# Kernel tuning notes

Hardware: AMD Instinct MI355X
Metric: run time of the kernel (lower is better)

The kernel has to match this reference:

```python
import jax, jax.numpy as jnp
import numpy as np

B, T, N = 64, 100, 20000
ALPHA, BETA = 1.0, 0.5  # ExpRelu params


def setup_inputs() -> dict:
    rng = np.random.default_rng(0)
    # Proper SE(3) poses so the inverse is well-conditioned
    A = rng.normal(size=(B, 3, 3))
    Q, _ = np.linalg.qr(A)
    det = np.linalg.det(Q)
    Q[:, :, 0] *= det[:, None]  # force det(R) = +1
    poses = np.tile(np.eye(4, dtype=np.float64), (B, 1, 1))
    poses[:, :3, :3] = Q
    poses[:, :3, 3] = rng.normal(size=(B, 3)) * 10.0
    # Homogeneous global boundary points [4, N]
    pts = rng.normal(size=(3, N)) * 50.0
    boundary = np.concatenate([pts, np.ones((1, N))], axis=0)
    # Unit boundary normals [3, N]
    nrm = rng.normal(size=(3, N))
    nrm /= np.linalg.norm(nrm, axis=0, keepdims=True)
    # Local-frame waypoints [B, T, 3]
    wpts = rng.normal(size=(B, T, 3)) * 5.0
    return {
        "posesglobal": jnp.asarray(poses, dtype=jnp.float32),
        "waypointslocal": jnp.asarray(wpts, dtype=jnp.float32),
        "boundary": jnp.asarray(boundary, dtype=jnp.float32),
        "boundarynormals": jnp.asarray(nrm, dtype=jnp.float32),
    }


def _exp_relu(x):
    return jnp.where(x > 0.0, ALPHA * x + 1.0, jnp.exp(BETA * x))


def reference(posesglobal, waypointslocal, boundary, boundarynormals):
    posesinv = jnp.linalg.inv(posesglobal)                     # [B,4,4]
    # boundary points into each local frame: [B,N,3]
    bpl = jnp.einsum("bij,jn->bni", posesinv, boundary)[..., :3]
    # rotate normals into local frame: [B,N,3]
    bnl = jnp.einsum("bij,jn->bni", posesinv[:, :3, :3], boundarynormals)
    # 1-NN search: squared distances [B,T,N] (argmin-equivalent to cdist)
    w2 = jnp.sum(waypointslocal * waypointslocal, axis=-1)     # [B,T]
    p2 = jnp.sum(bpl * bpl, axis=-1)                           # [B,N]
    cross = jnp.einsum("btd,bnd->btn", waypointslocal, bpl)    # [B,T,N]
    d2 = w2[:, :, None] + p2[:, None, :] - 2.0 * cross
    idx = jnp.argmin(d2, axis=2)                               # [B,T]
    cp = jnp.take_along_axis(bpl, idx[..., None], axis=1)      # [B,T,3]
    cn = jnp.take_along_axis(bnl, idx[..., None], axis=1)      # [B,T,3]
    dots = jnp.sum((waypointslocal - cp) * cn, axis=2)         # [B,T]
    loss = jnp.mean(jnp.mean(_exp_relu(dots), axis=1))         # scalar
    return loss
```

## Files before the change

kernel.cpp:

```cpp
#include <hip/hip_runtime.h>
#include <math.h>
#include <float.h>

#define B_ 64
#define T_ 100
#define N_ 20000
#define NQ (B_ * T_)
#define NCHUNKS 100
#define CHUNK (N_ / NCHUNKS)
#define PAIRS (CHUNK / 2)
#define GROUPS (PAIRS / 2)
#define QG 256
#define NQG (NQ / QG)
#define K1_THREADS 128

typedef float f2 __attribute__((ext_vector_type(2)));
typedef float f4 __attribute__((ext_vector_type(4)));
typedef unsigned long long u64;

#define KEYS_OFF 0

__device__ __forceinline__ unsigned int f32_sortable(float f) {
    unsigned int u = __float_as_uint(f);
    return ((int)u >= 0) ? (u | 0x80000000u) : ~u;
}

__global__ __launch_bounds__(256) void k0_init(u64* __restrict__ keys,
                                               float* __restrict__ out)
{
    const int i = blockIdx.x * 256 + threadIdx.x;
    keys[i] = ~0ull;
    if (i == 0) out[0] = 0.0f;
}

__global__ __launch_bounds__(K1_THREADS) void k1_nn(
    const float* __restrict__ poses,
    const float* __restrict__ wpts,
    const float* __restrict__ boundary,
    u64* __restrict__ keys)
{
    __shared__ f4 sh[PAIRS][2];
    const int bx   = blockIdx.x;
    const int qg   = bx / NCHUNKS;
    const int c    = bx - qg * NCHUNKS;
    const int base = c * CHUNK;
    const int tid  = threadIdx.x;

    if (tid < PAIRS) {
        const int p  = tid;
        const int n0 = base + 2 * p;
        const float x0 = boundary[n0],          x1 = boundary[n0 + 1];
        const float y0 = boundary[N_ + n0],     y1 = boundary[N_ + n0 + 1];
        const float z0 = boundary[2 * N_ + n0], z1 = boundary[2 * N_ + n0 + 1];
        f4 a = { -2.f * x0, -2.f * x1, -2.f * y0, -2.f * y1 };
        f4 b = { -2.f * z0, -2.f * z1,
                 x0 * x0 + y0 * y0 + z0 * z0,
                 x1 * x1 + y1 * y1 + z1 * z1 };
        sh[p][0] = a;
        sh[p][1] = b;
    }

    const int i0 = qg * QG + tid;
    const int i1 = i0 + K1_THREADS;

    float q0x, q0y, q0z, q1x, q1y, q1z;
    {
        int b0 = i0 / T_;
        const float* P = poses + b0 * 16;
        const float* W = wpts + i0 * 3;
        float wx = W[0], wy = W[1], wz = W[2];
        q0x = P[0] * wx + P[1] * wy + P[2]  * wz + P[3];
        q0y = P[4] * wx + P[5] * wy + P[6]  * wz + P[7];
        q0z = P[8] * wx + P[9] * wy + P[10] * wz + P[11];
    }
    {
        int b1 = i1 / T_;
        const float* P = poses + b1 * 16;
        const float* W = wpts + i1 * 3;
        float wx = W[0], wy = W[1], wz = W[2];
        q1x = P[0] * wx + P[1] * wy + P[2]  * wz + P[3];
        q1y = P[4] * wx + P[5] * wy + P[6]  * wz + P[7];
        q1z = P[8] * wx + P[9] * wy + P[10] * wz + P[11];
    }
    __syncthreads();

    const f2 v0x = { q0x, q0x }, v0y = { q0y, q0y }, v0z = { q0z, q0z };
    const f2 v1x = { q1x, q1x }, v1y = { q1y, q1y }, v1z = { q1z, q1z };

    float best0 = FLT_MAX, best1 = FLT_MAX;
    int   bg0 = 0, bg1 = 0;

#pragma unroll 5
    for (int g = 0; g < GROUPS; ++g) {
        const f4 a0 = sh[2 * g][0],     b0 = sh[2 * g][1];
        const f4 a1 = sh[2 * g + 1][0], b1 = sh[2 * g + 1][1];
        const f2 mx0 = { a0.x, a0.y }, my0 = { a0.z, a0.w };
        const f2 mz0 = { b0.x, b0.y }, p20 = { b0.z, b0.w };
        const f2 mx1 = { a1.x, a1.y }, my1 = { a1.z, a1.w };
        const f2 mz1 = { b1.x, b1.y }, p21 = { b1.z, b1.w };

        f2 eA = __builtin_elementwise_fma(mx0, v0x,
                __builtin_elementwise_fma(my0, v0y,
                __builtin_elementwise_fma(mz0, v0z, p20)));
        f2 eB = __builtin_elementwise_fma(mx1, v0x,
                __builtin_elementwise_fma(my1, v0y,
                __builtin_elementwise_fma(mz1, v0z, p21)));
        float m0 = fminf(fminf(eA.x, eA.y), fminf(eB.x, eB.y));
        if (m0 < best0) { best0 = m0; bg0 = g; }

        f2 eC = __builtin_elementwise_fma(mx0, v1x,
                __builtin_elementwise_fma(my0, v1y,
                __builtin_elementwise_fma(mz0, v1z, p20)));
        f2 eD = __builtin_elementwise_fma(mx1, v1x,
                __builtin_elementwise_fma(my1, v1y,
                __builtin_elementwise_fma(mz1, v1z, p21)));
        float m1 = fminf(fminf(eC.x, eC.y), fminf(eD.x, eD.y));
        if (m1 < best1) { best1 = m1; bg1 = g; }
    }

    {
        const f4 a0 = sh[2 * bg0][0],     b0 = sh[2 * bg0][1];
        const f4 a1 = sh[2 * bg0 + 1][0], b1 = sh[2 * bg0 + 1][1];
        const f2 mx0 = { a0.x, a0.y }, my0 = { a0.z, a0.w };
        const f2 mz0 = { b0.x, b0.y }, p20 = { b0.z, b0.w };
        const f2 mx1 = { a1.x, a1.y }, my1 = { a1.z, a1.w };
        const f2 mz1 = { b1.x, b1.y }, p21 = { b1.z, b1.w };
        f2 eA = __builtin_elementwise_fma(mx0, v0x,
                __builtin_elementwise_fma(my0, v0y,
                __builtin_elementwise_fma(mz0, v0z, p20)));
        f2 eB = __builtin_elementwise_fma(mx1, v0x,
                __builtin_elementwise_fma(my1, v0y,
                __builtin_elementwise_fma(mz1, v0z, p21)));
        int loc = 4 * bg0;
        int li = (eA.x == best0) ? loc
               : (eA.y == best0) ? loc + 1
               : (eB.x == best0) ? loc + 2 : loc + 3;
        u64 key = ((u64)f32_sortable(best0) << 32) | (unsigned)(base + li);
        atomicMin(&keys[i0], key);
    }
    {
        const f4 a0 = sh[2 * bg1][0],     b0 = sh[2 * bg1][1];
        const f4 a1 = sh[2 * bg1 + 1][0], b1 = sh[2 * bg1 + 1][1];
        const f2 mx0 = { a0.x, a0.y }, my0 = { a0.z, a0.w };
        const f2 mz0 = { b0.x, b0.y }, p20 = { b0.z, b0.w };
        const f2 mx1 = { a1.x, a1.y }, my1 = { a1.z, a1.w };
        const f2 mz1 = { b1.x, b1.y }, p21 = { b1.z, b1.w };
        f2 eC = __builtin_elementwise_fma(mx0, v1x,
                __builtin_elementwise_fma(my0, v1y,
                __builtin_elementwise_fma(mz0, v1z, p20)));
        f2 eD = __builtin_elementwise_fma(mx1, v1x,
                __builtin_elementwise_fma(my1, v1y,
                __builtin_elementwise_fma(mz1, v1z, p21)));
        int loc = 4 * bg1;
        int li = (eC.x == best1) ? loc
               : (eC.y == best1) ? loc + 1
               : (eD.x == best1) ? loc + 2 : loc + 3;
        u64 key = ((u64)f32_sortable(best1) << 32) | (unsigned)(base + li);
        atomicMin(&keys[i1], key);
    }
}

__global__ __launch_bounds__(256) void k2_epilogue(
    const float* __restrict__ poses,
    const float* __restrict__ wpts,
    const float* __restrict__ boundary,
    const float* __restrict__ bnorm,
    const u64* __restrict__ keys,
    float* __restrict__ out)
{
    const int tid = threadIdx.x;
    const int i = blockIdx.x * 256 + tid;

    const int bi = (int)(unsigned)(keys[i] & 0xFFFFFFFFull);

    const int b = i / T_;
    const float* P = poses + b * 16;
    const float* W = wpts + i * 3;
    const float wx = W[0], wy = W[1], wz = W[2];
    const float qx = P[0] * wx + P[1] * wy + P[2]  * wz + P[3];
    const float qy = P[4] * wx + P[5] * wy + P[6]  * wz + P[7];
    const float qz = P[8] * wx + P[9] * wy + P[10] * wz + P[11];

    const float gx = boundary[bi], gy = boundary[N_ + bi], gz = boundary[2 * N_ + bi];
    const float nx = bnorm[bi],    ny = bnorm[N_ + bi],    nz = bnorm[2 * N_ + bi];

    const float dots = (qx - gx) * nx + (qy - gy) * ny + (qz - gz) * nz;
    float val = (dots > 0.0f) ? (dots + 1.0f) : expf(0.5f * dots);
    val *= (1.0f / (float)NQ);

    __shared__ float red[256];
    red[tid] = val;
    __syncthreads();
#pragma unroll
    for (int s = 128; s > 0; s >>= 1) {
        if (tid < s) red[tid] += red[tid + s];
        __syncthreads();
    }
    if (tid == 0) atomicAdd(out, red[0]);
}

extern "C" void kernel_launch(void* const* d_in, const int* in_sizes, int n_in,
                              void* d_out, int out_size, void* d_ws, size_t ws_size,
                              hipStream_t stream) {
    const float* poses    = (const float*)d_in[0];
    const float* wpts     = (const float*)d_in[1];
    const float* boundary = (const float*)d_in[2];
    const float* bnorm    = (const float*)d_in[3];
    float* out = (float*)d_out;

    u64* keys = (u64*)((char*)d_ws + KEYS_OFF);

    k0_init<<<NQ / 256, 256, 0, stream>>>(keys, out);
    k1_nn<<<NQG * NCHUNKS, K1_THREADS, 0, stream>>>(
        poses, wpts, boundary, keys);
    k2_epilogue<<<NQ / 256, 256, 0, stream>>>(
        poses, wpts, boundary, bnorm, keys, out);
}
```

Baseline: 81.00 us.

## Precompute packed boundary points globally and read them uniformly instead of via LDS

Packing of boundary points into the (-2x,-2y,-2z,|p|^2) layout moves into the prep kernel, which writes it once to workspace and keeps the key and output initialisation. The NN kernel then reads the chunk straight from global memory with wave-uniform addresses, which can become scalar or broadcast loads, and drops the LDS staging and its __syncthreads. The intent is to remove the per-block LDS fill and ds_read traffic from the inner loop. The cost is reliance on the cache for every point read, an extra workspace buffer, and a changed unroll factor.

```diff
diff --git a/kernel.cpp b/kernel.cpp
--- a/kernel.cpp
+++ b/kernel.cpp
@@ -8,8 +8,9 @@
 #define NQ (B_ * T_)
 #define NCHUNKS 100
 #define CHUNK (N_ / NCHUNKS)
-#define PAIRS (CHUNK / 2)
-#define GROUPS (PAIRS / 2)
+#define PAIRS_TOTAL (N_ / 2)
+#define CPAIRS (CHUNK / 2)
+#define GROUPS (CPAIRS / 2)
 #define QG 256
 #define NQG (NQ / QG)
 #define K1_THREADS 128
@@ -18,37 +19,23 @@
 typedef float f4 __attribute__((ext_vector_type(4)));
 typedef unsigned long long u64;
 
-#define KEYS_OFF 0
+#define PTS_OFF  0
+#define KEYS_OFF (2 * PAIRS_TOTAL * sizeof(f4))
 
 __device__ __forceinline__ unsigned int f32_sortable(float f) {
     unsigned int u = __float_as_uint(f);
     return ((int)u >= 0) ? (u | 0x80000000u) : ~u;
 }
 
-__global__ __launch_bounds__(256) void k0_init(u64* __restrict__ keys,
-                                               float* __restrict__ out)
+__global__ __launch_bounds__(256) void k0_prep(
+    const float* __restrict__ boundary,
+    f4* __restrict__ pts,
+    u64* __restrict__ keys,
+    float* __restrict__ out)
 {
     const int i = blockIdx.x * 256 + threadIdx.x;
-    keys[i] = ~0ull;
-    if (i == 0) out[0] = 0.0f;
-}
-
-__global__ __launch_bounds__(K1_THREADS) void k1_nn(
-    const float* __restrict__ poses,
-    const float* __restrict__ wpts,
-    const float* __restrict__ boundary,
-    u64* __restrict__ keys)
-{
-    __shared__ f4 sh[PAIRS][2];
-    const int bx   = blockIdx.x;
-    const int qg   = bx / NCHUNKS;
-    const int c    = bx - qg * NCHUNKS;
-    const int base = c * CHUNK;
-    const int tid  = threadIdx.x;
-
-    if (tid < PAIRS) {
-        const int p  = tid;
-        const int n0 = base + 2 * p;
+    if (i < PAIRS_TOTAL) {
+        const int n0 = 2 * i;
         const float x0 = boundary[n0],          x1 = boundary[n0 + 1];
         const float y0 = boundary[N_ + n0],     y1 = boundary[N_ + n0 + 1];
         const float z0 = boundary[2 * N_ + n0], z1 = boundary[2 * N_ + n0 + 1];
@@ -56,9 +43,26 @@
         f4 b = { -2.f * z0, -2.f * z1,
                  x0 * x0 + y0 * y0 + z0 * z0,
                  x1 * x1 + y1 * y1 + z1 * z1 };
-        sh[p][0] = a;
-        sh[p][1] = b;
-    }
+        pts[2 * i]     = a;
+        pts[2 * i + 1] = b;
+    }
+    if (i < NQ) keys[i] = ~0ull;
+    if (i == 0) out[0] = 0.0f;
+}
+
+__global__ __launch_bounds__(K1_THREADS) void k1_nn(
+    const float* __restrict__ poses,
+    const float* __restrict__ wpts,
+    const f4* __restrict__ pts,
+    u64* __restrict__ keys)
+{
+    const int bx   = blockIdx.x;
+    const int qg   = bx / NCHUNKS;
+    const int c    = bx - qg * NCHUNKS;
+    const int base = c * CHUNK;
+    const int tid  = threadIdx.x;
+
+    const f4* __restrict__ pp = pts + 2 * (c * CPAIRS);
 
     const int i0 = qg * QG + tid;
     const int i1 = i0 + K1_THREADS;
@@ -82,7 +86,6 @@
         q1y = P[4] * wx + P[5] * wy + P[6]  * wz + P[7];
         q1z = P[8] * wx + P[9] * wy + P[10] * wz + P[11];
     }
-    __syncthreads();
 
     const f2 v0x = { q0x, q0x }, v0y = { q0y, q0y }, v0z = { q0z, q0z };
     const f2 v1x = { q1x, q1x }, v1y = { q1y, q1y }, v1z = { q1z, q1z };
@@ -90,10 +93,10 @@
     float best0 = FLT_MAX, best1 = FLT_MAX;
     int   bg0 = 0, bg1 = 0;
 
-#pragma unroll 5
+#pragma unroll 4
     for (int g = 0; g < GROUPS; ++g) {
-        const f4 a0 = sh[2 * g][0],     b0 = sh[2 * g][1];
-        const f4 a1 = sh[2 * g + 1][0], b1 = sh[2 * g + 1][1];
+        const f4 a0 = pp[4 * g + 0], b0 = pp[4 * g + 1];
+        const f4 a1 = pp[4 * g + 2], b1 = pp[4 * g + 3];
         const f2 mx0 = { a0.x, a0.y }, my0 = { a0.z, a0.w };
         const f2 mz0 = { b0.x, b0.y }, p20 = { b0.z, b0.w };
         const f2 mx1 = { a1.x, a1.y }, my1 = { a1.z, a1.w };
@@ -119,8 +122,8 @@
     }
 
     {
-        const f4 a0 = sh[2 * bg0][0],     b0 = sh[2 * bg0][1];
-        const f4 a1 = sh[2 * bg0 + 1][0], b1 = sh[2 * bg0 + 1][1];
+        const f4 a0 = pp[4 * bg0 + 0], b0 = pp[4 * bg0 + 1];
+        const f4 a1 = pp[4 * bg0 + 2], b1 = pp[4 * bg0 + 3];
         const f2 mx0 = { a0.x, a0.y }, my0 = { a0.z, a0.w };
         const f2 mz0 = { b0.x, b0.y }, p20 = { b0.z, b0.w };
         const f2 mx1 = { a1.x, a1.y }, my1 = { a1.z, a1.w };
@@ -139,8 +142,8 @@
         atomicMin(&keys[i0], key);
     }
     {
-        const f4 a0 = sh[2 * bg1][0],     b0 = sh[2 * bg1][1];
-        const f4 a1 = sh[2 * bg1 + 1][0], b1 = sh[2 * bg1 + 1][1];
+        const f4 a0 = pp[4 * bg1 + 0], b0 = pp[4 * bg1 + 1];
+        const f4 a1 = pp[4 * bg1 + 2], b1 = pp[4 * bg1 + 3];
         const f2 mx0 = { a0.x, a0.y }, my0 = { a0.z, a0.w };
         const f2 mz0 = { b0.x, b0.y }, p20 = { b0.z, b0.w };
         const f2 mx1 = { a1.x, a1.y }, my1 = { a1.z, a1.w };
@@ -208,11 +211,13 @@
     const float* bnorm    = (const float*)d_in[3];
     float* out = (float*)d_out;
 
+    f4*  pts  = (f4*)((char*)d_ws + PTS_OFF);
     u64* keys = (u64*)((char*)d_ws + KEYS_OFF);
 
-    k0_init<<<NQ / 256, 256, 0, stream>>>(keys, out);
+    k0_prep<<<(PAIRS_TOTAL + 255) / 256, 256, 0, stream>>>(
+        boundary, pts, keys, out);
     k1_nn<<<NQG * NCHUNKS, K1_THREADS, 0, stream>>>(
-        poses, wpts, boundary, keys);
+        poses, wpts, pts, keys);
     k2_epilogue<<<NQ / 256, 256, 0, stream>>>(
         poses, wpts, boundary, bnorm, keys, out);
 }
```

Result: slower. 83.52 us (+3.1%).

## Register-block ten queries per thread in NN search and stage poses in LDS

Applied to the files above, without the earlier changes.

The nearest-neighbour kernel now gives each thread 10 queries instead of 2 and uses 64-thread blocks with smaller boundary chunks (80 points). Each LDS read of boundary data is therefore reused across more queries. Poses are staged in shared memory, and the per-group argmin update is written as branch-free selects. The init kernel is replaced by hipMemsetAsync calls. The trade-off is higher register pressure, fewer threads per block, and more atomicMin traffic from more chunks.

```diff
diff --git a/kernel.cpp b/kernel.cpp
--- a/kernel.cpp
+++ b/kernel.cpp
@@ -6,13 +6,14 @@
 #define T_ 100
 #define N_ 20000
 #define NQ (B_ * T_)
-#define NCHUNKS 100
+#define NCHUNKS 250
 #define CHUNK (N_ / NCHUNKS)
-#define PAIRS (CHUNK / 2)
-#define GROUPS (PAIRS / 2)
-#define QG 256
+#define CPAIRS (CHUNK / 2)
+#define GROUPS (CPAIRS / 2)
+#define QG 640
 #define NQG (NQ / QG)
-#define K1_THREADS 128
+#define QPT 10
+#define K1_THREADS 64
 
 typedef float f2 __attribute__((ext_vector_type(2)));
 typedef float f4 __attribute__((ext_vector_type(4)));
@@ -25,30 +26,31 @@
     return ((int)u >= 0) ? (u | 0x80000000u) : ~u;
 }
 
-__global__ __launch_bounds__(256) void k0_init(u64* __restrict__ keys,
-                                               float* __restrict__ out)
-{
-    const int i = blockIdx.x * 256 + threadIdx.x;
-    keys[i] = ~0ull;
-    if (i == 0) out[0] = 0.0f;
-}
-
 __global__ __launch_bounds__(K1_THREADS) void k1_nn(
     const float* __restrict__ poses,
     const float* __restrict__ wpts,
     const float* __restrict__ boundary,
     u64* __restrict__ keys)
 {
-    __shared__ f4 sh[PAIRS][2];
+    __shared__ f4 sh[GROUPS][4];
+    __shared__ float sposes[B_ * 16];
+
     const int bx   = blockIdx.x;
     const int qg   = bx / NCHUNKS;
     const int c    = bx - qg * NCHUNKS;
     const int base = c * CHUNK;
     const int tid  = threadIdx.x;
 
-    if (tid < PAIRS) {
-        const int p  = tid;
-        const int n0 = base + 2 * p;
+    {
+        const f4* pg  = (const f4*)poses;
+        f4*       sp4 = (f4*)sposes;
+#pragma unroll
+        for (int j = 0; j < 4; ++j)
+            sp4[j * 64 + tid] = pg[j * 64 + tid];
+    }
+
+    if (tid < CPAIRS) {
+        const int n0 = base + 2 * tid;
         const float x0 = boundary[n0],          x1 = boundary[n0 + 1];
         const float y0 = boundary[N_ + n0],     y1 = boundary[N_ + n0 + 1];
         const float z0 = boundary[2 * N_ + n0], z1 = boundary[2 * N_ + n0 + 1];
@@ -56,107 +58,82 @@
         f4 b = { -2.f * z0, -2.f * z1,
                  x0 * x0 + y0 * y0 + z0 * z0,
                  x1 * x1 + y1 * y1 + z1 * z1 };
-        sh[p][0] = a;
-        sh[p][1] = b;
-    }
-
-    const int i0 = qg * QG + tid;
-    const int i1 = i0 + K1_THREADS;
-
-    float q0x, q0y, q0z, q1x, q1y, q1z;
-    {
-        int b0 = i0 / T_;
-        const float* P = poses + b0 * 16;
-        const float* W = wpts + i0 * 3;
-        float wx = W[0], wy = W[1], wz = W[2];
-        q0x = P[0] * wx + P[1] * wy + P[2]  * wz + P[3];
-        q0y = P[4] * wx + P[5] * wy + P[6]  * wz + P[7];
-        q0z = P[8] * wx + P[9] * wy + P[10] * wz + P[11];
-    }
-    {
-        int b1 = i1 / T_;
-        const float* P = poses + b1 * 16;
-        const float* W = wpts + i1 * 3;
-        float wx = W[0], wy = W[1], wz = W[2];
-        q1x = P[0] * wx + P[1] * wy + P[2]  * wz + P[3];
-        q1y = P[4] * wx + P[5] * wy + P[6]  * wz + P[7];
-        q1z = P[8] * wx + P[9] * wy + P[10] * wz + P[11];
+        sh[tid >> 1][(tid & 1) * 2 + 0] = a;
+        sh[tid >> 1][(tid & 1) * 2 + 1] = b;
     }
     __syncthreads();
 
-    const f2 v0x = { q0x, q0x }, v0y = { q0y, q0y }, v0z = { q0z, q0z };
-    const f2 v1x = { q1x, q1x }, v1y = { q1y, q1y }, v1z = { q1z, q1z };
-
-    float best0 = FLT_MAX, best1 = FLT_MAX;
-    int   bg0 = 0, bg1 = 0;
-
-#pragma unroll 5
-    for (int g = 0; g < GROUPS; ++g) {
-        const f4 a0 = sh[2 * g][0],     b0 = sh[2 * g][1];
-        const f4 a1 = sh[2 * g + 1][0], b1 = sh[2 * g + 1][1];
-        const f2 mx0 = { a0.x, a0.y }, my0 = { a0.z, a0.w };
-        const f2 mz0 = { b0.x, b0.y }, p20 = { b0.z, b0.w };
-        const f2 mx1 = { a1.x, a1.y }, my1 = { a1.z, a1.w };
-        const f2 mz1 = { b1.x, b1.y }, p21 = { b1.z, b1.w };
-
-        f2 eA = __builtin_elementwise_fma(mx0, v0x,
-                __builtin_elementwise_fma(my0, v0y,
-                __builtin_elementwise_fma(mz0, v0z, p20)));
-        f2 eB = __builtin_elementwise_fma(mx1, v0x,
-                __builtin_elementwise_fma(my1, v0y,
-                __builtin_elementwise_fma(mz1, v0z, p21)));
-        float m0 = fminf(fminf(eA.x, eA.y), fminf(eB.x, eB.y));
-        if (m0 < best0) { best0 = m0; bg0 = g; }
-
-        f2 eC = __builtin_elementwise_fma(mx0, v1x,
-                __builtin_elementwise_fma(my0, v1y,
-                __builtin_elementwise_fma(mz0, v1z, p20)));
-        f2 eD = __builtin_elementwise_fma(mx1, v1x,
-                __builtin_elementwise_fma(my1, v1y,
-                __builtin_elementwise_fma(mz1, v1z, p21)));
-        float m1 = fminf(fminf(eC.x, eC.y), fminf(eD.x, eD.y));
-        if (m1 < best1) { best1 = m1; bg1 = g; }
+    float qx[QPT], qy[QPT], qz[QPT];
+#pragma unroll
+    for (int k = 0; k < QPT; ++k) {
+        const int i = qg * QG + k * 64 + tid;
+        const int b = i / T_;
+        const float* P = sposes + b * 16;
+        const float* W = wpts + i * 3;
+        const float wx = W[0], wy = W[1], wz = W[2];
+        qx[k] = P[0] * wx + P[1] * wy + P[2]  * wz + P[3];
+        qy[k] = P[4] * wx + P[5] * wy + P[6]  * wz + P[7];
+        qz[k] = P[8] * wx + P[9] * wy + P[10] * wz + P[11];
     }
 
-    {
-        const f4 a0 = sh[2 * bg0][0],     b0 = sh[2 * bg0][1];
-        const f4 a1 = sh[2 * bg0 + 1][0], b1 = sh[2 * bg0 + 1][1];
-        const f2 mx0 = { a0.x, a0.y }, my0 = { a0.z, a0.w };
-        const f2 mz0 = { b0.x, b0.y }, p20 = { b0.z, b0.w };
-        const f2 mx1 = { a1.x, a1.y }, my1 = { a1.z, a1.w };
-        const f2 mz1 = { b1.x, b1.y }, p21 = { b1.z, b1.w };
-        f2 eA = __builtin_elementwise_fma(mx0, v0x,
-                __builtin_elementwise_fma(my0, v0y,
-                __builtin_elementwise_fma(mz0, v0z, p20)));
-        f2 eB = __builtin_elementwise_fma(mx1, v0x,
-                __builtin_elementwise_fma(my1, v0y,
-                __builtin_elementwise_fma(mz1, v0z, p21)));
-        int loc = 4 * bg0;
-        int li = (eA.x == best0) ? loc
-               : (eA.y == best0) ? loc + 1
-               : (eB.x == best0) ? loc + 2 : loc + 3;
-        u64 key = ((u64)f32_sortable(best0) << 32) | (unsigned)(base + li);
-        atomicMin(&keys[i0], key);
+    float beste[QPT];
+    int   bg[QPT];
+#pragma unroll
+    for (int k = 0; k < QPT; ++k) { beste[k] = FLT_MAX; bg[k] = 0; }
+
+#pragma unroll 4
+    for (int g = 0; g < GROUPS; ++g) {
+        const f4 A0 = sh[g][0], B0 = sh[g][1];
+        const f4 A1 = sh[g][2], B1 = sh[g][3];
+        const f2 mx0 = { A0.x, A0.y }, my0 = { A0.z, A0.w };
+        const f2 mz0 = { B0.x, B0.y }, p20 = { B0.z, B0.w };
+        const f2 mx1 = { A1.x, A1.y }, my1 = { A1.z, A1.w };
+        const f2 mz1 = { B1.x, B1.y }, p21 = { B1.z, B1.w };
+
+#pragma unroll
+        for (int k = 0; k < QPT; ++k) {
+            const f2 vx = { qx[k], qx[k] };
+            const f2 vy = { qy[k], qy[k] };
+            const f2 vz = { qz[k], qz[k] };
+            f2 eA = __builtin_elementwise_fma(mx0, vx,
+                    __builtin_elementwise_fma(my0, vy,
+                    __builtin_elementwise_fma(mz0, vz, p20)));
+            f2 eB = __builtin_elementwise_fma(mx1, vx,
+                    __builtin_elementwise_fma(my1, vy,
+                    __builtin_elementwise_fma(mz1, vz, p21)));
+            f2 m2 = __builtin_elementwise_min(eA, eB);
+            float m = fminf(m2.x, m2.y);
+            const bool cc = m < beste[k];
+            beste[k] = cc ? m : beste[k];
+            bg[k]    = cc ? g : bg[k];
+        }
     }
-    {
-        const f4 a0 = sh[2 * bg1][0],     b0 = sh[2 * bg1][1];
-        const f4 a1 = sh[2 * bg1 + 1][0], b1 = sh[2 * bg1 + 1][1];
-        const f2 mx0 = { a0.x, a0.y }, my0 = { a0.z, a0.w };
-        const f2 mz0 = { b0.x, b0.y }, p20 = { b0.z, b0.w };
-        const f2 mx1 = { a1.x, a1.y }, my1 = { a1.z, a1.w };
-        const f2 mz1 = { b1.x, b1.y }, p21 = { b1.z, b1.w };
-        f2 eC = __builtin_elementwise_fma(mx0, v1x,
-                __builtin_elementwise_fma(my0, v1y,
-                __builtin_elementwise_fma(mz0, v1z, p20)));
-        f2 eD = __builtin_elementwise_fma(mx1, v1x,
-                __builtin_elementwise_fma(my1, v1y,
-                __builtin_elementwise_fma(mz1, v1z, p21)));
-        int loc = 4 * bg1;
-        int li = (eC.x == best1) ? loc
-               : (eC.y == best1) ? loc + 1
-               : (eD.x == best1) ? loc + 2 : loc + 3;
-        u64 key = ((u64)f32_sortable(best1) << 32) | (unsigned)(base + li);
-        atomicMin(&keys[i1], key);
+
+#pragma unroll
+    for (int k = 0; k < QPT; ++k) {
+        const int g = bg[k];
+        const f4 A0 = sh[g][0], B0 = sh[g][1];
+        const f4 A1 = sh[g][2], B1 = sh[g][3];
+        const f2 mx0 = { A0.x, A0.y }, my0 = { A0.z, A0.w };
+        const f2 mz0 = { B0.x, B0.y }, p20 = { B0.z, B0.w };
+        const f2 mx1 = { A1.x, A1.y }, my1 = { A1.z, A1.w };
+        const f2 mz1 = { B1.x, B1.y }, p21 = { B1.z, B1.w };
+        const f2 vx = { qx[k], qx[k] };
+        const f2 vy = { qy[k], qy[k] };
+        const f2 vz = { qz[k], qz[k] };
+        f2 eA = __builtin_elementwise_fma(mx0, vx,
+                __builtin_elementwise_fma(my0, vy,
+                __builtin_elementwise_fma(mz0, vz, p20)));
+        f2 eB = __builtin_elementwise_fma(mx1, vx,
+                __builtin_elementwise_fma(my1, vy,
+                __builtin_elementwise_fma(mz1, vz, p21)));
+        const int loc = base + 4 * g;
+        const int li = (eA.x == beste[k]) ? loc
+                     : (eA.y == beste[k]) ? loc + 1
+                     : (eB.x == beste[k]) ? loc + 2 : loc + 3;
+        const u64 key = ((u64)f32_sortable(beste[k]) << 32) | (unsigned)li;
+        const int i = qg * QG + k * 64 + tid;
+        atomicMin(&keys[i], key);
     }
 }
 
@@ -210,7 +187,9 @@
 
     u64* keys = (u64*)((char*)d_ws + KEYS_OFF);
 
-    k0_init<<<NQ / 256, 256, 0, stream>>>(keys, out);
+    hipMemsetAsync(keys, 0xFF, NQ * sizeof(u64), stream);
+    hipMemsetAsync(out, 0, sizeof(float), stream);
+
     k1_nn<<<NQG * NCHUNKS, K1_THREADS, 0, stream>>>(
         poses, wpts, boundary, keys);
     k2_epilogue<<<NQ / 256, 256, 0, stream>>>(
```

After: 85.87 us. 6.0% more time.
